# Kernel optimization log

Hardware: AMD Instinct MI355X
Metric: run time of the kernel (lower is better)

Reference implementation:

```python
import jax, jax.numpy as jnp
import numpy as np

B, T, D = 512, 128, 256
L, CH, CS = 3, 128, 10
H = L * CH            # hidden_dim = 384
G = 4 * H + 2 * L     # gate projection width = 1542
HS = H // 6           # 64


def setup_inputs() -> dict:
    key = jax.random.key(0)
    ks = jax.random.split(key, 12)
    def lin(k, out_d, in_d):
        return jax.random.normal(k, (out_d, in_d), jnp.float32) * (1.0 / np.sqrt(in_d))
    return {
        "x": jax.random.normal(ks[0], (B, T, D), jnp.float32),
        "time": jax.random.uniform(ks[1], (B, T), jnp.float32),
        "kW": lin(ks[2], G, D + 1), "kb": jnp.zeros((G,), jnp.float32),
        "rW": lin(ks[3], G, H + 1), "rb": jnp.zeros((G,), jnp.float32),
        "sW": lin(ks[4], HS, H), "sb": jnp.zeros((HS,), jnp.float32),
        "rsW": lin(ks[5], H, HS), "rsb": jnp.zeros((H,), jnp.float32),
        "cW": lin(ks[6], H, H * CS).reshape(H, H, CS), "cb": jnp.zeros((H,), jnp.float32),
    }


def _cumax_l2r(z):
    return jnp.cumsum(jax.nn.softmax(z, axis=-1), axis=-1)


def _cumax_r2l(z):
    zf = jnp.flip(z, -1)
    return jnp.flip(jnp.cumsum(jax.nn.softmax(zf, axis=-1), axis=-1), -1)


def _forward(x, time, kW, kb, rW, rb, sW, sb, rsW, rsb, cW, cb):
    def step(carry, xt):
        c, h, buf_h, buf_d = carry
        xi, ti = xt                      # xi: (B,D), ti: (B,)
        ti = ti[:, None]
        xo = (jnp.concatenate([xi, ti], -1) @ kW.T + kb
              + jnp.concatenate([h, ti], -1) @ rW.T + rb)   # (B,G)
        fm = _cumax_l2r(xo[:, :L])[:, :, None]              # (B,L,1) master forget
        im = _cumax_r2l(xo[:, L:2 * L])[:, :, None]         # (B,L,1) master input
        g = xo[:, 2 * L:].reshape(-1, 4 * L, CH)
        fg = jax.nn.sigmoid(g[:, :L])
        ig = jax.nn.sigmoid(g[:, L:2 * L])
        og = jax.nn.sigmoid(g[:, 2 * L:3 * L])
        ci = jnp.tanh(g[:, 3 * L:])
        cl = c.reshape(-1, L, CH)
        ov = fm * im
        cn = ov * (fg * cl + ig * ci) + (fm - ov) * cl + (im - ov) * ci
        hn = og * jnp.tanh(cn)
        c_flat = cn.reshape(-1, H)
        h_flat = hn.reshape(-1, H)
        cur_dis = 1.0 - jnp.mean(fm[..., 0], axis=-1)       # (B,)
        buf_h = jnp.concatenate([buf_h[1:], h_flat[None]], 0)   # (CS,B,H)
        buf_d = jnp.concatenate([buf_d[1:], cur_dis[None]], 0)  # (CS,B)
        local_dis = jax.nn.softmax(jnp.cumsum(buf_d.T, axis=1), axis=1)  # (B,CS)
        local_h = buf_h.transpose(1, 2, 0) * local_dis[:, None, :]       # (B,H,CS)
        theme = jnp.mean(local_h, axis=-1)                               # (B,H)
        theme = jax.nn.sigmoid(jax.nn.relu(theme @ sW.T + sb) @ rsW.T + rsb)
        conv = jnp.einsum('bck,ock->bo', local_h, cW) + cb   # Conv1d over full window
        local = theme * conv
        return (c_flat, h_flat, buf_h, buf_d), (h_flat, local, cur_dis)

    z = jnp.zeros((x.shape[0], H), jnp.float32)
    carry0 = (z, z,
              jnp.zeros((CS, x.shape[0], H), jnp.float32),
              jnp.zeros((CS, x.shape[0]), jnp.float32))
    _, (origin_h, hs, dist) = jax.lax.scan(
        step, carry0, (x.transpose(1, 0, 2), time.T))
    output = hs.transpose(1, 0, 2) + origin_h.transpose(1, 0, 2)  # (B,T,H)
    last_output = output[:, -1, :]
    return last_output, output, dist  # dist: (T,B)


def reference(x, time, kW, kb, rW, rb, sW, sb, rsW, rsb, cW, cb):
    return _forward(x, time, kW, kb, rW, rb, sW, sb, rsW, rsb, cW, cb)
```

## Files before the change

### kernel.cpp

```cpp
#include <hip/hip_runtime.h>
#include <math.h>

typedef unsigned short u16;
typedef __attribute__((ext_vector_type(8))) short bf16x8;
typedef __attribute__((ext_vector_type(4))) float f32x4;

#define MFMA(a, b, c) __builtin_amdgcn_mfma_f32_16x16x32_bf16(a, b, c, 0, 0, 0)

#define Bsz 512
#define Tsz 128
#define Dsz 256
#define CSs 10
#define Hsz 384
#define Gsz 1542
#define HSz 64
#define Gp  1568
#define BG  ((size_t)Bsz * Gp)
#define NGT 98
#define KTH 12
#define KTX 8
#define KTC 120

constexpr size_t O_WPK  = 0;
constexpr size_t O_XWPK = O_WPK  + 2ull*NGT*KTH*2*512;
constexpr size_t O_CPK  = O_XWPK + 2ull*NGT*KTX*2*512;
constexpr size_t O_SPK  = O_CPK  + 2ull*24*KTC*512;
constexpr size_t O_RPK  = O_SPK  + 2ull*4*KTH*2*512;
constexpr size_t O_BC   = O_RPK  + 2ull*24*2*2*512;
constexpr size_t O_WT   = O_BC + 4ull*Gp;
constexpr size_t O_HBF  = (O_WT + 4ull*Gp + 255) & ~(size_t)255;
constexpr size_t O_XPK  = O_HBF + 2ull*Bsz*Tsz*Hsz;
constexpr size_t O_XWB  = O_XPK + 2ull*Tsz*32*KTX*2*512;
constexpr size_t O_HWB  = O_XWB + 4ull*2*BG;
constexpr size_t O_CFB  = O_HWB + 4ull*2*BG;
constexpr size_t ZERO_BEG = O_CFB;
constexpr size_t ZERO_END = O_CFB + 4ull*2*Bsz*Hsz;
constexpr size_t O_XWALL = (ZERO_END + 255) & ~(size_t)255;
constexpr size_t NEED_ALL = O_XWALL + 4ull*Tsz*BG;

__device__ __forceinline__ u16 f2bf(float f) {
    unsigned u = __float_as_uint(f);
    unsigned r = (u + 0x7FFFu + ((u >> 16) & 1u)) >> 16;
    return (u16)r;
}
__device__ __forceinline__ float bf2f(u16 v) {
    return __uint_as_float(((unsigned)v) << 16);
}
__device__ __forceinline__ float sigm(float v) { return 1.f / (1.f + expf(-v)); }

__global__ __launch_bounds__(256) void zero4(float4* __restrict__ p, int n4) {
    int i = blockIdx.x * 256 + threadIdx.x;
    if (i < n4) p[i] = make_float4(0.f, 0.f, 0.f, 0.f);
}

__global__ __launch_bounds__(256) void build_w(const float* __restrict__ kW,
                                               const float* __restrict__ kb,
                                               const float* __restrict__ rW,
                                               const float* __restrict__ rb,
                                               const float* __restrict__ sW,
                                               const float* __restrict__ rsW,
                                               u16* __restrict__ wpk,
                                               u16* __restrict__ xwpk,
                                               u16* __restrict__ spk,
                                               u16* __restrict__ rpk,
                                               float* __restrict__ bc,
                                               float* __restrict__ wt) {
    const int N1 = Gp * 384, N2 = Gp * 256, N3 = 64 * 384, N4 = 384 * 64;
    int idx = blockIdx.x * 256 + threadIdx.x;
    if (idx < N1) {
        int g = idx / 384, k = idx % 384;
        float v = (g < Gsz) ? rW[g * (Hsz + 1) + k] : 0.f;
        u16 hi = f2bf(v), lo = f2bf(v - bf2f(hi));
        size_t fo = ((size_t)((g >> 4) * KTH + (k >> 5)) * 2) * 512;
        int pos = ((g & 15) | (((k >> 3) & 3) << 4)) * 8 + (k & 7);
        wpk[fo + pos] = hi; wpk[fo + 512 + pos] = lo;
    } else if (idx < N1 + N2) {
        int i = idx - N1;
        int g = i / 256, k = i % 256;
        float v = (g < Gsz) ? kW[g * (Dsz + 1) + k] : 0.f;
        u16 hi = f2bf(v), lo = f2bf(v - bf2f(hi));
        size_t fo = ((size_t)((g >> 4) * KTX + (k >> 5)) * 2) * 512;
        int pos = ((g & 15) | (((k >> 3) & 3) << 4)) * 8 + (k & 7);
        xwpk[fo + pos] = hi; xwpk[fo + 512 + pos] = lo;
    } else if (idx < N1 + N2 + N3) {
        int i = idx - N1 - N2;
        int g = i / 384, k = i % 384;
        float v = sW[g * Hsz + k];
        u16 hi = f2bf(v), lo = f2bf(v - bf2f(hi));
        size_t fo = ((size_t)((g >> 4) * KTH + (k >> 5)) * 2) * 512;
        int pos = ((g & 15) | (((k >> 3) & 3) << 4)) * 8 + (k & 7);
        spk[fo + pos] = hi; spk[fo + 512 + pos] = lo;
    } else if (idx < N1 + N2 + N3 + N4) {
        int i = idx - N1 - N2 - N3;
        int g = i / 64, k = i % 64;
        float v = rsW[g * HSz + k];
        u16 hi = f2bf(v), lo = f2bf(v - bf2f(hi));
        size_t fo = ((size_t)((g >> 4) * 2 + (k >> 5)) * 2) * 512;
        int pos = ((g & 15) | (((k >> 3) & 3) << 4)) * 8 + (k & 7);
        rpk[fo + pos] = hi; rpk[fo + 512 + pos] = lo;
    } else if (idx < N1 + N2 + N3 + N4 + Gsz) {
        int g = idx - N1 - N2 - N3 - N4;
        bc[g] = kb[g] + rb[g];
        wt[g] = kW[g * (Dsz + 1) + Dsz] + rW[g * (Hsz + 1) + Hsz];
    }
}

__global__ __launch_bounds__(256) void pack_x(const float* __restrict__ x,
                                              u16* __restrict__ xpk) {
    int idx = blockIdx.x * 256 + threadIdx.x;
    int k = idx & 255, b = (idx >> 8) & 511, t = idx >> 17;
    float v = x[((size_t)b * Tsz + t) * Dsz + k];
    u16 hi = f2bf(v), lo = f2bf(v - bf2f(hi));
    size_t fo = (((size_t)t * 32 + (b >> 4)) * KTX + (k >> 5)) * 2 * 512;
    int pos = ((b & 15) | (((k >> 3) & 3) << 4)) * 8 + (k & 7);
    xpk[fo + pos] = hi;
    xpk[fo + 512 + pos] = lo;
}

__global__ __launch_bounds__(256) void pack_cw(const float* __restrict__ cW,
                                               u16* __restrict__ cpk) {
    int idx = blockIdx.x * 256 + threadIdx.x;
    if (idx >= Hsz * Hsz * CSs) return;
    int o = idx / (Hsz * CSs), kk = idx % (Hsz * CSs);
    int ch = kk / CSs, jj = kk % CSs;
    int k2 = jj * Hsz + ch;
    size_t fo = ((size_t)(o >> 4) * KTC + (k2 >> 5)) * 512;
    int pos = ((o & 15) | (((k2 >> 3) & 3) << 4)) * 8 + (k2 & 7);
    cpk[fo + pos] = f2bf(cW[idx]);
}

__device__ __forceinline__ void xw_slab(const u16* __restrict__ xwpk,
                                        const u16* __restrict__ xpk,
                                        float* __restrict__ dst,
                                        int t, int mt, int sbp,
                                        int wave, int lane, int l15, int lk) {
    int base = sbp * 12 + (sbp < 2 ? sbp : 2);
    int cnt  = (sbp < 2) ? 13 : 12;
    const u16* Asrc = xpk + ((size_t)(t * 32 + mt) * KTX * 2) * 512;
    bf16x8 ah[KTX], al[KTX];
    #pragma unroll
    for (int kt = 0; kt < KTX; ++kt) {
        ah[kt] = *(const bf16x8*)(Asrc + (size_t)(kt * 2) * 512 + lane * 8);
        al[kt] = *(const bf16x8*)(Asrc + (size_t)(kt * 2 + 1) * 512 + lane * 8);
    }
    #pragma unroll
    for (int ti = 0; ti < 2; ++ti) {
        int idx = 2 * wave + ti;
        if (idx < cnt) {
            int gt = base + idx;
            f32x4 acc = {};
            #pragma unroll
            for (int half = 0; half < 2; ++half) {
                bf16x8 bh[4], bl[4];
                #pragma unroll
                for (int kk = 0; kk < 4; ++kk) {
                    int kt = half * 4 + kk;
                    size_t fb = ((size_t)(gt * KTX + kt) * 2) * 512 + lane * 8;
                    bh[kk] = *(const bf16x8*)(xwpk + fb);
                    bl[kk] = *(const bf16x8*)(xwpk + fb + 512);
                }
                #pragma unroll
                for (int kk = 0; kk < 4; ++kk) {
                    int kt = half * 4 + kk;
                    acc = MFMA(ah[kt], bh[kk], acc);
                    acc = MFMA(ah[kt], bl[kk], acc);
                    acc = MFMA(al[kt], bh[kk], acc);
                }
            }
            int col = gt * 16 + l15;
            #pragma unroll
            for (int j = 0; j < 4; ++j)
                dst[(size_t)(mt * 16 + lk * 4 + j) * Gp + col] = acc[j];
        }
    }
}

__global__ __launch_bounds__(448) void xwall_k(char* __restrict__ ws) {
    const u16* xwpk = (const u16*)(ws + O_XWPK);
    const u16* xpk  = (const u16*)(ws + O_XPK);
    float* xwall = (float*)(ws + O_XWALL);
    int q = blockIdx.x, t = blockIdx.y;
    int mt = q >> 3, sbp = q & 7;
    int wave = threadIdx.x >> 6, lane = threadIdx.x & 63;
    xw_slab(xwpk, xpk, xwall + (size_t)t * BG, t, mt, sbp,
            wave, lane, lane & 15, lane >> 4);
}

__global__ __launch_bounds__(448) void fused(const float* __restrict__ tme,
                                             char* __restrict__ ws,
                                             float* __restrict__ out, int t,
                                             int use_all) {
    const u16* wpk  = (const u16*)(ws + O_WPK);
    const u16* xwpk = (const u16*)(ws + O_XWPK);
    const u16* xpk  = (const u16*)(ws + O_XPK);
    const float* bc = (const float*)(ws + O_BC);
    const float* wt = (const float*)(ws + O_WT);
    float* xw = (float*)(ws + O_XWB);
    float* hw = (float*)(ws + O_HWB);
    float* cf = (float*)(ws + O_CFB);
    u16* hbf = (u16*)(ws + O_HBF);
    float* out_seq  = out + (size_t)Bsz * Hsz;
    float* out_dist = out_seq + (size_t)Bsz * Tsz * Hsz;

    int bid = blockIdx.x;
    int tid = threadIdx.x;
    int wave = tid >> 6, lane = tid & 63, l15 = lane & 15, lk = lane >> 4;
    int role = bid >> 8;
    int q = bid & 255;
    int mt = q >> 3, sbp = q & 7;

    __shared__ u16 s_h[KTH][2][512];
    __shared__ float s_fi[16][4];

    if (role == 1) {
        if (t >= Tsz) return;
        float* dst = xw + (size_t)(t & 1) * BG;
        xw_slab(xwpk, xpk, dst, t, mt, sbp, wave, lane, l15, lk);
        return;
    }
    if (sbp == 7) return;

    if (t == 0) {
        for (int i = tid; i < KTH * 2 * 256; i += 448) ((unsigned*)s_h)[i] = 0u;
    } else {
        const float* xw1 = use_all ? (const float*)(ws + O_XWALL) + (size_t)(t - 1) * BG
                                   : xw + (size_t)((t - 1) & 1) * BG;
        const float* hw1 = hw + (size_t)((t - 1) & 1) * BG;
        const float* cfo = cf + (size_t)(t & 1) * Bsz * Hsz;
        float* cfn = cf + (size_t)((t - 1) & 1) * Bsz * Hsz;
        if (tid < 16) {
            int r = tid, b = mt * 16 + r;
            float tv = tme[b * Tsz + (t - 1)];
            const float* xr = xw1 + (size_t)b * Gp;
            const float* hr = hw1 + (size_t)b * Gp;
            float zf[6];
            #pragma unroll
            for (int g = 0; g < 6; ++g)
                zf[g] = xr[g] + hr[g] + bc[g] + tv * wt[g];
            float m = fmaxf(zf[0], fmaxf(zf[1], zf[2]));
            float e0 = expf(zf[0] - m), e1 = expf(zf[1] - m), e2 = expf(zf[2] - m);
            float inv = 1.f / (e0 + e1 + e2);
            float fm0 = e0 * inv, fm1 = fm0 + e1 * inv;
            float mw = fmaxf(zf[3], fmaxf(zf[4], zf[5]));
            float f0 = expf(zf[3] - mw), f1 = expf(zf[4] - mw), f2 = expf(zf[5] - mw);
            float invw = 1.f / (f0 + f1 + f2);
            float im2 = f2 * invw, im1 = f1 * invw + im2;
            s_fi[r][0] = fm0; s_fi[r][1] = fm1; s_fi[r][2] = im1; s_fi[r][3] = im2;
            if (sbp == 0)
                out_dist[(size_t)(t - 1) * Bsz + b] = 1.f - (fm0 + fm1 + 1.f) * (1.f / 3.f);
        }
        __syncthreads();
        if (tid < Hsz) {
            int ch = tid;
            int l = ch >> 7;
            int kt = ch >> 5;
            int g0 = 6 + ch, g1 = g0 + Hsz, g2 = g0 + 2 * Hsz, g3 = g0 + 3 * Hsz;
            float bcg0 = bc[g0], bcg1 = bc[g1], bcg2 = bc[g2], bcg3 = bc[g3];
            float wtg0 = wt[g0], wtg1 = wt[g1], wtg2 = wt[g2], wtg3 = wt[g3];
            const float* xr = xw1 + (size_t)(mt * 16) * Gp;
            const float* hr = hw1 + (size_t)(mt * 16) * Gp;
            float nx0 = xr[g0], nx1 = xr[g1], nx2 = xr[g2], nx3 = xr[g3];
            float nh0 = hr[g0], nh1 = hr[g1], nh2 = hr[g2], nh3 = hr[g3];
            for (int r = 0; r < 16; ++r) {
                float cx0 = nx0, cx1 = nx1, cx2 = nx2, cx3 = nx3;
                float hv0 = nh0, hv1 = nh1, hv2 = nh2, hv3 = nh3;
                if (r < 15) {
                    const float* xr2 = xr + (size_t)(r + 1) * Gp;
                    const float* hr2 = hr + (size_t)(r + 1) * Gp;
                    nx0 = xr2[g0]; nx1 = xr2[g1]; nx2 = xr2[g2]; nx3 = xr2[g3];
                    nh0 = hr2[g0]; nh1 = hr2[g1]; nh2 = hr2[g2]; nh3 = hr2[g3];
                }
                int b = mt * 16 + r;
                float tv = tme[b * Tsz + (t - 1)];
                float fm = (l == 0) ? s_fi[r][0] : ((l == 1) ? s_fi[r][1] : 1.f);
                float im = (l == 0) ? 1.f : ((l == 1) ? s_fi[r][2] : s_fi[r][3]);
                float fg = sigm(cx0 + hv0 + bcg0 + tv * wtg0);
                float ig = sigm(cx1 + hv1 + bcg1 + tv * wtg1);
                float og = sigm(cx2 + hv2 + bcg2 + tv * wtg2);
                float ci = tanhf(cx3 + hv3 + bcg3 + tv * wtg3);
                float cl = cfo[(size_t)b * Hsz + ch];
                float ov = fm * im;
                float cn = ov * (fg * cl + ig * ci) + (fm - ov) * cl + (im - ov) * ci;
                float hn = og * tanhf(cn);
                u16 hh = f2bf(hn);
                u16 hl = f2bf(hn - bf2f(hh));
                if (sbp == 0) {
                    cfn[(size_t)b * Hsz + ch] = cn;
                    size_t oi = ((size_t)b * Tsz + (t - 1)) * Hsz + ch;
                    out_seq[oi] = hn;
                    hbf[oi] = hh;
                }
                int pos = (r | (((ch >> 3) & 3) << 4)) * 8 + (ch & 7);
                s_h[kt][0][pos] = hh;
                s_h[kt][1][pos] = hl;
            }
        }
    }
    __syncthreads();
    if (t >= Tsz) return;

    float* dst = hw + (size_t)(t & 1) * BG;
    #pragma unroll
    for (int ti = 0; ti < 2; ++ti) {
        int gt = sbp * 14 + wave * 2 + ti;
        f32x4 acc = {};
        #pragma unroll
        for (int half = 0; half < 2; ++half) {
            bf16x8 bh[6], bl[6];
            #pragma unroll
            for (int kk = 0; kk < 6; ++kk) {
                int kt = half * 6 + kk;
                size_t fb = ((size_t)(gt * KTH + kt) * 2) * 512 + lane * 8;
                bh[kk] = *(const bf16x8*)(wpk + fb);
                bl[kk] = *(const bf16x8*)(wpk + fb + 512);
            }
            #pragma unroll
            for (int kk = 0; kk < 6; ++kk) {
                int kt = half * 6 + kk;
                bf16x8 ah = *(const bf16x8*)&s_h[kt][0][lane * 8];
                bf16x8 al = *(const bf16x8*)&s_h[kt][1][lane * 8];
                acc = MFMA(ah, bh[kk], acc);
                acc = MFMA(ah, bl[kk], acc);
                acc = MFMA(al, bh[kk], acc);
            }
        }
        int col = gt * 16 + l15;
        #pragma unroll
        for (int j = 0; j < 4; ++j)
            dst[(size_t)(mt * 16 + lk * 4 + j) * Gp + col] = acc[j];
    }
}

__global__ __launch_bounds__(512, 1) void post(const float* __restrict__ sb,
                                               const float* __restrict__ rsb,
                                               const float* __restrict__ cb,
                                               char* __restrict__ ws,
                                               float* __restrict__ out) {
    const u16* cpk = (const u16*)(ws + O_CPK);
    const u16* spk = (const u16*)(ws + O_SPK);
    const u16* rpk = (const u16*)(ws + O_RPK);
    const u16* hbf = (const u16*)(ws + O_HBF);

    float* out_last = out;
    float* out_seq  = out + (size_t)Bsz * Hsz;
    const float* out_dist = out_seq + (size_t)Bsz * Tsz * Hsz;

    int b = blockIdx.x, t0 = blockIdx.y * 16;
    int tid = threadIdx.x;
    int wave = tid >> 6, lane = tid & 63, l15 = lane & 15, lk = lane >> 4;

    __shared__ u16 s_apk[KTC][512];
    __shared__ u16 s_tpk[KTH * 2][512];
    __shared__ float th1s[16][68];
    __shared__ float s_ld[16][CSs];

    if (tid < 16) {
        int r = tid;
        float vals[CSs];
        float cum = 0.f;
        #pragma unroll
        for (int j = 0; j < CSs; ++j) {
            int tp = t0 + r - 9 + j;
            float d = (tp < 0) ? 0.f : out_dist[(size_t)tp * Bsz + b];
            cum += d;
            vals[j] = cum;
        }
        float mx = vals[0];
        #pragma unroll
        for (int j = 1; j < CSs; ++j) mx = fmaxf(mx, vals[j]);
        float sum = 0.f;
        #pragma unroll
        for (int j = 0; j < CSs; ++j) { vals[j] = expf(vals[j] - mx); sum += vals[j]; }
        float invs = 1.f / sum;
        #pragma unroll
        for (int j = 0; j < CSs; ++j) s_ld[r][j] = vals[j] * invs;
    }
    __syncthreads();

    for (int u = tid; u < 768; u += 512) {
        int c8 = u >> 4, r = u & 15;
        int ch0 = c8 * 8;
        int rowoff = c8 >> 2;
        int pos16 = (r | ((c8 & 3) << 4)) * 8;
        bf16x8 hv[CSs];
        #pragma unroll
        for (int j = 0; j < CSs; ++j) {
            int tp = t0 + r - 9 + j;
            bf16x8 z = {};
            hv[j] = (tp >= 0) ? *(const bf16x8*)(hbf + ((size_t)b * Tsz + tp) * Hsz + ch0) : z;
        }
        float acc[8] = {0.f, 0.f, 0.f, 0.f, 0.f, 0.f, 0.f, 0.f};
        #pragma unroll
        for (int j = 0; j < CSs; ++j) {
            float ldv = s_ld[r][j];
            bf16x8 av8;
            #pragma unroll
            for (int e = 0; e < 8; ++e) {
                float av = bf2f((u16)hv[j][e]) * ldv;
                acc[e] += av;
                av8[e] = (short)f2bf(av);
            }
            *(bf16x8*)&s_apk[j * 12 + rowoff][pos16] = av8;
        }
        bf16x8 th8, tl8;
        #pragma unroll
        for (int e = 0; e < 8; ++e) {
            float thm = acc[e] * 0.1f;
            u16 th = f2bf(thm);
            th8[e] = (short)th;
            tl8[e] = (short)f2bf(thm - bf2f(th));
        }
        int kt2 = rowoff * 2;
        *(bf16x8*)&s_tpk[kt2][pos16] = th8;
        *(bf16x8*)&s_tpk[kt2 + 1][pos16] = tl8;
    }
    __syncthreads();

    f32x4 cacc[3] = {};
    for (int k0 = 0; k0 < KTC; k0 += 8) {
        bf16x8 bv[3][8];
        #pragma unroll
        for (int kk = 0; kk < 8; ++kk)
            #pragma unroll
            for (int i = 0; i < 3; ++i)
                bv[i][kk] = *(const bf16x8*)(cpk + ((size_t)((wave * 3 + i) * KTC + k0 + kk)) * 512 + lane * 8);
        #pragma unroll
        for (int kk = 0; kk < 8; ++kk) {
            bf16x8 a = *(const bf16x8*)&s_apk[k0 + kk][lane * 8];
            #pragma unroll
            for (int i = 0; i < 3; ++i)
                cacc[i] = MFMA(a, bv[i][kk], cacc[i]);
        }
    }
    if (wave < 4) {
        f32x4 a1 = {};
        for (int kt = 0; kt < KTH; ++kt) {
            bf16x8 ah = *(const bf16x8*)&s_tpk[kt * 2][lane * 8];
            bf16x8 al = *(const bf16x8*)&s_tpk[kt * 2 + 1][lane * 8];
            size_t bb = ((size_t)(wave * KTH + kt) * 2) * 512 + lane * 8;
            bf16x8 bh = *(const bf16x8*)(spk + bb);
            bf16x8 bl = *(const bf16x8*)(spk + bb + 512);
            a1 = MFMA(ah, bh, a1);
            a1 = MFMA(ah, bl, a1);
            a1 = MFMA(al, bh, a1);
        }
        int col = wave * 16 + l15;
        #pragma unroll
        for (int j = 0; j < 4; ++j)
            th1s[lk * 4 + j][col] = fmaxf(a1[j] + sb[col], 0.f);
    }
    __syncthreads();

    bf16x8 ah2[2], al2[2];
    #pragma unroll
    for (int kt = 0; kt < 2; ++kt) {
        bf16x8 zh, zl;
        #pragma unroll
        for (int e = 0; e < 8; ++e) {
            float v = th1s[l15][kt * 32 + lk * 8 + e];
            u16 hi = f2bf(v);
            zh[e] = (short)hi;
            zl[e] = (short)f2bf(v - bf2f(hi));
        }
        ah2[kt] = zh; al2[kt] = zl;
    }
    #pragma unroll
    for (int i = 0; i < 3; ++i) {
        int ot = wave * 3 + i;
        f32x4 a2 = {};
        #pragma unroll
        for (int kt = 0; kt < 2; ++kt) {
            size_t bb = ((size_t)(ot * 2 + kt) * 2) * 512 + lane * 8;
            bf16x8 bh = *(const bf16x8*)(rpk + bb);
            bf16x8 bl = *(const bf16x8*)(rpk + bb + 512);
            a2 = MFMA(ah2[kt], bh, a2);
            a2 = MFMA(ah2[kt], bl, a2);
            a2 = MFMA(al2[kt], bh, a2);
        }
        int col = ot * 16 + l15;
        #pragma unroll
        for (int j = 0; j < 4; ++j) {
            int row = lk * 4 + j;
            int tt = t0 + row;
            size_t oi = ((size_t)b * Tsz + tt) * Hsz + col;
            float convv = cacc[i][j] + cb[col];
            float th = sigm(a2[j] + rsb[col]);
            float val = th * convv + out_seq[oi];
            out_seq[oi] = val;
            if (tt == Tsz - 1) out_last[(size_t)b * Hsz + col] = val;
        }
    }
}

extern "C" void kernel_launch(void* const* d_in, const int* in_sizes, int n_in,
                              void* d_out, int out_size, void* d_ws, size_t ws_size,
                              hipStream_t stream) {
    const float* x   = (const float*)d_in[0];
    const float* tme = (const float*)d_in[1];
    const float* kW  = (const float*)d_in[2];
    const float* kb  = (const float*)d_in[3];
    const float* rW  = (const float*)d_in[4];
    const float* rb  = (const float*)d_in[5];
    const float* sW  = (const float*)d_in[6];
    const float* sb  = (const float*)d_in[7];
    const float* rsW = (const float*)d_in[8];
    const float* rsb = (const float*)d_in[9];
    const float* cW  = (const float*)d_in[10];
    const float* cb  = (const float*)d_in[11];

    char* wsb = (char*)d_ws;
    float* outp = (float*)d_out;

    u16* wpk  = (u16*)(wsb + O_WPK);
    u16* xwpk = (u16*)(wsb + O_XWPK);
    u16* cpk  = (u16*)(wsb + O_CPK);
    u16* spk  = (u16*)(wsb + O_SPK);
    u16* rpk  = (u16*)(wsb + O_RPK);
    float* bc = (float*)(wsb + O_BC);
    float* wt = (float*)(wsb + O_WT);
    u16* xpk  = (u16*)(wsb + O_XPK);

    int use_all = (ws_size >= NEED_ALL) ? 1 : 0;

    zero4<<<(int)((ZERO_END - ZERO_BEG) / 16 + 255) / 256, 256, 0, stream>>>(
        (float4*)(wsb + ZERO_BEG), (int)((ZERO_END - ZERO_BEG) / 16));
    {
        int nW = Gp * 384 + Gp * 256 + 64 * 384 + 384 * 64 + Gsz;
        build_w<<<(nW + 255) / 256, 256, 0, stream>>>(kW, kb, rW, rb, sW, rsW,
                                                      wpk, xwpk, spk, rpk, bc, wt);
    }
    pack_x<<<(Tsz * Bsz * Dsz) / 256, 256, 0, stream>>>(x, xpk);
    pack_cw<<<(Hsz * Hsz * CSs + 255) / 256, 256, 0, stream>>>(cW, cpk);

    if (use_all)
        xwall_k<<<dim3(256, Tsz), 448, 0, stream>>>(wsb);

    int grid = use_all ? 256 : 512;
    for (int t = 0; t <= Tsz; ++t)
        fused<<<grid, 448, 0, stream>>>(tme, wsb, outp, t, use_all);
    post<<<dim3(Bsz, Tsz / 16), 512, 0, stream>>>(sb, rsb, cb, wsb, outp);
}
```

Measured before the change: 3.660 ms.

## Widen fused step blocks to 1024 threads and merge x-projection role

```diff
diff --git a/kernel.cpp b/kernel.cpp
--- a/kernel.cpp
+++ b/kernel.cpp
@@ -186,10 +186,10 @@
             wave, lane, lane & 15, lane >> 4);
 }
 
-__global__ __launch_bounds__(448) void fused(const float* __restrict__ tme,
-                                             char* __restrict__ ws,
-                                             float* __restrict__ out, int t,
-                                             int use_all) {
+__global__ __launch_bounds__(1024, 1) void fused(const float* __restrict__ tme,
+                                                 char* __restrict__ ws,
+                                                 float* __restrict__ out, int t,
+                                                 int use_all) {
     const u16* wpk  = (const u16*)(ws + O_WPK);
     const u16* xwpk = (const u16*)(ws + O_XWPK);
     const u16* xpk  = (const u16*)(ws + O_XPK);
@@ -205,129 +205,160 @@
     int bid = blockIdx.x;
     int tid = threadIdx.x;
     int wave = tid >> 6, lane = tid & 63, l15 = lane & 15, lk = lane >> 4;
-    int role = bid >> 8;
-    int q = bid & 255;
-    int mt = q >> 3, sbp = q & 7;
+    int mt = bid >> 3, sbp = bid & 7;
 
     __shared__ u16 s_h[KTH][2][512];
     __shared__ float s_fi[16][4];
 
-    if (role == 1) {
-        if (t >= Tsz) return;
-        float* dst = xw + (size_t)(t & 1) * BG;
-        xw_slab(xwpk, xpk, dst, t, mt, sbp, wave, lane, l15, lk);
-        return;
-    }
-    if (sbp == 7) return;
-
-    if (t == 0) {
-        for (int i = tid; i < KTH * 2 * 256; i += 448) ((unsigned*)s_h)[i] = 0u;
-    } else {
-        const float* xw1 = use_all ? (const float*)(ws + O_XWALL) + (size_t)(t - 1) * BG
-                                   : xw + (size_t)((t - 1) & 1) * BG;
-        const float* hw1 = hw + (size_t)((t - 1) & 1) * BG;
-        const float* cfo = cf + (size_t)(t & 1) * Bsz * Hsz;
-        float* cfn = cf + (size_t)((t - 1) & 1) * Bsz * Hsz;
-        if (tid < 16) {
-            int r = tid, b = mt * 16 + r;
-            float tv = tme[b * Tsz + (t - 1)];
-            const float* xr = xw1 + (size_t)b * Gp;
-            const float* hr = hw1 + (size_t)b * Gp;
-            float zf[6];
-            #pragma unroll
-            for (int g = 0; g < 6; ++g)
-                zf[g] = xr[g] + hr[g] + bc[g] + tv * wt[g];
-            float m = fmaxf(zf[0], fmaxf(zf[1], zf[2]));
-            float e0 = expf(zf[0] - m), e1 = expf(zf[1] - m), e2 = expf(zf[2] - m);
-            float inv = 1.f / (e0 + e1 + e2);
-            float fm0 = e0 * inv, fm1 = fm0 + e1 * inv;
-            float mw = fmaxf(zf[3], fmaxf(zf[4], zf[5]));
-            float f0 = expf(zf[3] - mw), f1 = expf(zf[4] - mw), f2 = expf(zf[5] - mw);
-            float invw = 1.f / (f0 + f1 + f2);
-            float im2 = f2 * invw, im1 = f1 * invw + im2;
-            s_fi[r][0] = fm0; s_fi[r][1] = fm1; s_fi[r][2] = im1; s_fi[r][3] = im2;
-            if (sbp == 0)
-                out_dist[(size_t)(t - 1) * Bsz + b] = 1.f - (fm0 + fm1 + 1.f) * (1.f / 3.f);
+    if (sbp < 7) {
+        if (t == 0) {
+            for (int i = tid; i < KTH * 2 * 256; i += 1024) ((unsigned*)s_h)[i] = 0u;
+        } else {
+            const float* xw1 = use_all ? (const float*)(ws + O_XWALL) + (size_t)(t - 1) * BG
+                                       : xw + (size_t)((t - 1) & 1) * BG;
+            const float* hw1 = hw + (size_t)((t - 1) & 1) * BG;
+            const float* cfo = cf + (size_t)(t & 1) * Bsz * Hsz;
+            float* cfn = cf + (size_t)((t - 1) & 1) * Bsz * Hsz;
+            if (tid < 16) {
+                int r = tid, b = mt * 16 + r;
+                float tv = tme[b * Tsz + (t - 1)];
+                const float* xr = xw1 + (size_t)b * Gp;
+                const float* hr = hw1 + (size_t)b * Gp;
+                float zf[6];
+                #pragma unroll
+                for (int g = 0; g < 6; ++g)
+                    zf[g] = xr[g] + hr[g] + bc[g] + tv * wt[g];
+                float m = fmaxf(zf[0], fmaxf(zf[1], zf[2]));
+                float e0 = expf(zf[0] - m), e1 = expf(zf[1] - m), e2 = expf(zf[2] - m);
+                float inv = 1.f / (e0 + e1 + e2);
+                float fm0 = e0 * inv, fm1 = fm0 + e1 * inv;
+                float mw = fmaxf(zf[3], fmaxf(zf[4], zf[5]));
+                float f0 = expf(zf[3] - mw), f1 = expf(zf[4] - mw), f2 = expf(zf[5] - mw);
+                float invw = 1.f / (f0 + f1 + f2);
+                float im2 = f2 * invw, im1 = f1 * invw + im2;
+                s_fi[r][0] = fm0; s_fi[r][1] = fm1; s_fi[r][2] = im1; s_fi[r][3] = im2;
+                if (sbp == 0)
+                    out_dist[(size_t)(t - 1) * Bsz + b] = 1.f - (fm0 + fm1 + 1.f) * (1.f / 3.f);
+            }
+            __syncthreads();
+            if (tid < 768) {
+                int ch = tid >> 1;
+                int rh = tid & 1;
+                int l = ch >> 7;
+                int kt = ch >> 5;
+                int g0 = 6 + ch, g1 = g0 + Hsz, g2 = g0 + 2 * Hsz, g3 = g0 + 3 * Hsz;
+                float bcg0 = bc[g0], bcg1 = bc[g1], bcg2 = bc[g2], bcg3 = bc[g3];
+                float wtg0 = wt[g0], wtg1 = wt[g1], wtg2 = wt[g2], wtg3 = wt[g3];
+                const float* xr = xw1 + (size_t)(mt * 16 + rh * 8) * Gp;
+                const float* hr = hw1 + (size_t)(mt * 16 + rh * 8) * Gp;
+                float nx0 = xr[g0], nx1 = xr[g1], nx2 = xr[g2], nx3 = xr[g3];
+                float nh0 = hr[g0], nh1 = hr[g1], nh2 = hr[g2], nh3 = hr[g3];
+                for (int r2 = 0; r2 < 8; ++r2) {
+                    float cx0 = nx0, cx1 = nx1, cx2 = nx2, cx3 = nx3;
+                    float hv0 = nh0, hv1 = nh1, hv2 = nh2, hv3 = nh3;
+                    if (r2 < 7) {
+                        const float* xr2 = xr + (size_t)(r2 + 1) * Gp;
+                        const float* hr2 = hr + (size_t)(r2 + 1) * Gp;
+                        nx0 = xr2[g0]; nx1 = xr2[g1]; nx2 = xr2[g2]; nx3 = xr2[g3];
+                        nh0 = hr2[g0]; nh1 = hr2[g1]; nh2 = hr2[g2]; nh3 = hr2[g3];
+                    }
+                    int r = rh * 8 + r2;
+                    int b = mt * 16 + r;
+                    float tv = tme[b * Tsz + (t - 1)];
+                    float fm = (l == 0) ? s_fi[r][0] : ((l == 1) ? s_fi[r][1] : 1.f);
+                    float im = (l == 0) ? 1.f : ((l == 1) ? s_fi[r][2] : s_fi[r][3]);
+                    float fg = sigm(cx0 + hv0 + bcg0 + tv * wtg0);
+                    float ig = sigm(cx1 + hv1 + bcg1 + tv * wtg1);
+                    float og = sigm(cx2 + hv2 + bcg2 + tv * wtg2);
+                    float ci = tanhf(cx3 + hv3 + bcg3 + tv * wtg3);
+                    float cl = cfo[(size_t)b * Hsz + ch];
+                    float ov = fm * im;
+                    float cn = ov * (fg * cl + ig * ci) + (fm - ov) * cl + (im - ov) * ci;
+                    float hn = og * tanhf(cn);
+                    u16 hh = f2bf(hn);
+                    u16 hl = f2bf(hn - bf2f(hh));
+                    if (sbp == 0) {
+                        cfn[(size_t)b * Hsz + ch] = cn;
+                        size_t oi = ((size_t)b * Tsz + (t - 1)) * Hsz + ch;
+                        out_seq[oi] = hn;
+                        hbf[oi] = hh;
+                    }
+                    int pos = (r | (((ch >> 3) & 3) << 4)) * 8 + (ch & 7);
+                    s_h[kt][0][pos] = hh;
+                    s_h[kt][1][pos] = hl;
+                }
+            }
         }
         __syncthreads();
-        if (tid < Hsz) {
-            int ch = tid;
-            int l = ch >> 7;
-            int kt = ch >> 5;
-            int g0 = 6 + ch, g1 = g0 + Hsz, g2 = g0 + 2 * Hsz, g3 = g0 + 3 * Hsz;
-            float bcg0 = bc[g0], bcg1 = bc[g1], bcg2 = bc[g2], bcg3 = bc[g3];
-            float wtg0 = wt[g0], wtg1 = wt[g1], wtg2 = wt[g2], wtg3 = wt[g3];
-            const float* xr = xw1 + (size_t)(mt * 16) * Gp;
-            const float* hr = hw1 + (size_t)(mt * 16) * Gp;
-            float nx0 = xr[g0], nx1 = xr[g1], nx2 = xr[g2], nx3 = xr[g3];
-            float nh0 = hr[g0], nh1 = hr[g1], nh2 = hr[g2], nh3 = hr[g3];
-            for (int r = 0; r < 16; ++r) {
-                float cx0 = nx0, cx1 = nx1, cx2 = nx2, cx3 = nx3;
-                float hv0 = nh0, hv1 = nh1, hv2 = nh2, hv3 = nh3;
-                if (r < 15) {
-                    const float* xr2 = xr + (size_t)(r + 1) * Gp;
-                    const float* hr2 = hr + (size_t)(r + 1) * Gp;
-                    nx0 = xr2[g0]; nx1 = xr2[g1]; nx2 = xr2[g2]; nx3 = xr2[g3];
-                    nh0 = hr2[g0]; nh1 = hr2[g1]; nh2 = hr2[g2]; nh3 = hr2[g3];
-                }
-                int b = mt * 16 + r;
-                float tv = tme[b * Tsz + (t - 1)];
-                float fm = (l == 0) ? s_fi[r][0] : ((l == 1) ? s_fi[r][1] : 1.f);
-                float im = (l == 0) ? 1.f : ((l == 1) ? s_fi[r][2] : s_fi[r][3]);
-                float fg = sigm(cx0 + hv0 + bcg0 + tv * wtg0);
-                float ig = sigm(cx1 + hv1 + bcg1 + tv * wtg1);
-                float og = sigm(cx2 + hv2 + bcg2 + tv * wtg2);
-                float ci = tanhf(cx3 + hv3 + bcg3 + tv * wtg3);
-                float cl = cfo[(size_t)b * Hsz + ch];
-                float ov = fm * im;
-                float cn = ov * (fg * cl + ig * ci) + (fm - ov) * cl + (im - ov) * ci;
-                float hn = og * tanhf(cn);
-                u16 hh = f2bf(hn);
-                u16 hl = f2bf(hn - bf2f(hh));
-                if (sbp == 0) {
-                    cfn[(size_t)b * Hsz + ch] = cn;
-                    size_t oi = ((size_t)b * Tsz + (t - 1)) * Hsz + ch;
-                    out_seq[oi] = hn;
-                    hbf[oi] = hh;
-                }
-                int pos = (r | (((ch >> 3) & 3) << 4)) * 8 + (ch & 7);
-                s_h[kt][0][pos] = hh;
-                s_h[kt][1][pos] = hl;
-            }
-        }
-    }
-    __syncthreads();
-    if (t >= Tsz) return;
-
-    float* dst = hw + (size_t)(t & 1) * BG;
-    #pragma unroll
-    for (int ti = 0; ti < 2; ++ti) {
-        int gt = sbp * 14 + wave * 2 + ti;
-        f32x4 acc = {};
-        #pragma unroll
-        for (int half = 0; half < 2; ++half) {
-            bf16x8 bh[6], bl[6];
-            #pragma unroll
-            for (int kk = 0; kk < 6; ++kk) {
-                int kt = half * 6 + kk;
-                size_t fb = ((size_t)(gt * KTH + kt) * 2) * 512 + lane * 8;
-                bh[kk] = *(const bf16x8*)(wpk + fb);
-                bl[kk] = *(const bf16x8*)(wpk + fb + 512);
-            }
-            #pragma unroll
-            for (int kk = 0; kk < 6; ++kk) {
-                int kt = half * 6 + kk;
-                bf16x8 ah = *(const bf16x8*)&s_h[kt][0][lane * 8];
-                bf16x8 al = *(const bf16x8*)&s_h[kt][1][lane * 8];
-                acc = MFMA(ah, bh[kk], acc);
-                acc = MFMA(ah, bl[kk], acc);
-                acc = MFMA(al, bh[kk], acc);
-            }
-        }
-        int col = gt * 16 + l15;
-        #pragma unroll
-        for (int j = 0; j < 4; ++j)
-            dst[(size_t)(mt * 16 + lk * 4 + j) * Gp + col] = acc[j];
+
+        if (t < Tsz && wave < 14) {
+            int gt = sbp * 14 + wave;
+            float* dst = hw + (size_t)(t & 1) * BG;
+            f32x4 acc = {};
+            #pragma unroll
+            for (int half = 0; half < 2; ++half) {
+                bf16x8 bh[6], bl[6];
+                #pragma unroll
+                for (int kk = 0; kk < 6; ++kk) {
+                    int kt = half * 6 + kk;
+                    size_t fb = ((size_t)(gt * KTH + kt) * 2) * 512 + lane * 8;
+                    bh[kk] = *(const bf16x8*)(wpk + fb);
+                    bl[kk] = *(const bf16x8*)(wpk + fb + 512);
+                }
+                #pragma unroll
+                for (int kk = 0; kk < 6; ++kk) {
+                    int kt = half * 6 + kk;
+                    bf16x8 ah = *(const bf16x8*)&s_h[kt][0][lane * 8];
+                    bf16x8 al = *(const bf16x8*)&s_h[kt][1][lane * 8];
+                    acc = MFMA(ah, bh[kk], acc);
+                    acc = MFMA(ah, bl[kk], acc);
+                    acc = MFMA(al, bh[kk], acc);
+                }
+            }
+            int col = gt * 16 + l15;
+            #pragma unroll
+            for (int j = 0; j < 4; ++j)
+                dst[(size_t)(mt * 16 + lk * 4 + j) * Gp + col] = acc[j];
+        }
+    }
+
+    if (!use_all && t < Tsz) {
+        int base = sbp * 12 + (sbp < 2 ? sbp : 2);
+        int cnt  = (sbp < 2) ? 13 : 12;
+        if (wave < cnt) {
+            int gt = base + wave;
+            const u16* Asrc = xpk + ((size_t)(t * 32 + mt) * KTX * 2) * 512;
+            bf16x8 ah[KTX], al[KTX];
+            #pragma unroll
+            for (int kt = 0; kt < KTX; ++kt) {
+                ah[kt] = *(const bf16x8*)(Asrc + (size_t)(kt * 2) * 512 + lane * 8);
+                al[kt] = *(const bf16x8*)(Asrc + (size_t)(kt * 2 + 1) * 512 + lane * 8);
+            }
+            float* dst = xw + (size_t)(t & 1) * BG;
+            f32x4 acc = {};
+            #pragma unroll
+            for (int half = 0; half < 2; ++half) {
+                bf16x8 bh[4], bl[4];
+                #pragma unroll
+                for (int kk = 0; kk < 4; ++kk) {
+                    int kt = half * 4 + kk;
+                    size_t fb = ((size_t)(gt * KTX + kt) * 2) * 512 + lane * 8;
+                    bh[kk] = *(const bf16x8*)(xwpk + fb);
+                    bl[kk] = *(const bf16x8*)(xwpk + fb + 512);
+                }
+                #pragma unroll
+                for (int kk = 0; kk < 4; ++kk) {
+                    int kt = half * 4 + kk;
+                    acc = MFMA(ah[kt], bh[kk], acc);
+                    acc = MFMA(ah[kt], bl[kk], acc);
+                    acc = MFMA(al[kt], bh[kk], acc);
+                }
+            }
+            int col = gt * 16 + l15;
+            #pragma unroll
+            for (int j = 0; j < 4; ++j)
+                dst[(size_t)(mt * 16 + lk * 4 + j) * Gp + col] = acc[j];
+        }
     }
 }
 
@@ -535,8 +566,7 @@
     if (use_all)
         xwall_k<<<dim3(256, Tsz), 448, 0, stream>>>(wsb);
 
-    int grid = use_all ? 256 : 512;
     for (int t = 0; t <= Tsz; ++t)
-        fused<<<grid, 448, 0, stream>>>(tme, wsb, outp, t, use_all);
+        fused<<<256, 1024, 0, stream>>>(tme, wsb, outp, t, use_all);
     post<<<dim3(Bsz, Tsz / 16), 512, 0, stream>>>(sb, rsb, cb, wsb, outp);
 }
```

Result: faster. 3.580 ms (-2.2%).
